# Kernel tuning notes

Hardware: AMD Instinct MI355X
Metric: run time of the kernel (lower is better)

The kernel has to match this reference:

```python
import jax, jax.numpy as jnp
import numpy as np

ALPHA = 0.5

def setup_inputs() -> dict:
    key = jax.random.key(0)
    k1, k2 = jax.random.split(key)
    B, S, F_IN, F_OUT = 64, 512, 1024, 1024
    x = jax.random.normal(k1, (B, S, F_IN), dtype=jnp.float32)
    W = jax.random.normal(k2, (F_OUT, F_IN), dtype=jnp.float32) * (F_IN ** -0.5)
    return {"x": x, "W": W}

def reference(x, W):
    # x: [B, S, F_in], W: [F_out, F_in] (torch Linear layout, no bias)
    alpha = jnp.asarray(ALPHA, dtype=x.dtype)
    # Project all segments at once (the big GEMM), then scan the EMA recurrence.
    y = jnp.einsum('bsf,of->bso', x, W)  # [B, S, F_out]
    y_t = jnp.swapaxes(y, 0, 1)          # [S, B, F_out] for scan over segments

    def step(h, yk):
        h = alpha * h + (1 - alpha) * yk
        return h, h

    h0 = jnp.zeros((x.shape[0], W.shape[0]), dtype=x.dtype)
    hk, hiddens_t = jax.lax.scan(step, h0, y_t)
    hiddens = jnp.swapaxes(hiddens_t, 0, 1)  # [B, S, F_out]
    return (hk, hiddens)
```

## Files before the change

kernel.cpp:

```cpp
#include <hip/hip_runtime.h>
#include <hip/hip_bf16.h>
#include <stdint.h>

#define B_DIM 64
#define S_DIM 512
#define K_DIM 1024
#define N_DIM 1024
#define M_DIM (B_DIM * S_DIM)

typedef __attribute__((ext_vector_type(8))) short short8;
typedef __attribute__((ext_vector_type(4))) float floatx4;

__global__ __launch_bounds__(256) void scan_x_kernel(
    const float* __restrict__ x, __hip_bfloat16* __restrict__ xs) {
  const int t  = blockIdx.x * 256 + threadIdx.x;
  const int f4 = (t & 255) << 2;
  const int c  = (t >> 8) & 15;
  const int b  = t >> 12;
  const size_t base = (size_t)b * S_DIM * K_DIM + f4;
  const int s0 = c * 32;

  float4 h = {0.f, 0.f, 0.f, 0.f};
  if (c != 0) {
    #pragma unroll 8
    for (int s = s0 - 16; s < s0; ++s) {
      float4 v = *(const float4*)(x + base + (size_t)s * K_DIM);
      h.x = 0.5f * (h.x + v.x); h.y = 0.5f * (h.y + v.y);
      h.z = 0.5f * (h.z + v.z); h.w = 0.5f * (h.w + v.w);
    }
  }
  #pragma unroll 8
  for (int s = s0; s < s0 + 32; ++s) {
    float4 v = *(const float4*)(x + base + (size_t)s * K_DIM);
    h.x = 0.5f * (h.x + v.x); h.y = 0.5f * (h.y + v.y);
    h.z = 0.5f * (h.z + v.z); h.w = 0.5f * (h.w + v.w);
    __hip_bfloat16 b0 = __float2bfloat16(h.x);
    __hip_bfloat16 b1 = __float2bfloat16(h.y);
    __hip_bfloat16 b2 = __float2bfloat16(h.z);
    __hip_bfloat16 b3 = __float2bfloat16(h.w);
    union { unsigned short u[4]; uint2 v2; } pk;
    pk.u[0] = *(unsigned short*)&b0; pk.u[1] = *(unsigned short*)&b1;
    pk.u[2] = *(unsigned short*)&b2; pk.u[3] = *(unsigned short*)&b3;
    *(uint2*)(xs + base + (size_t)s * K_DIM) = pk.v2;
  }
}

__global__ __launch_bounds__(256) void conv_w_kernel(
    const float* __restrict__ W, __hip_bfloat16* __restrict__ Wb) {
  int t = blockIdx.x * 256 + threadIdx.x;
  Wb[t] = __float2bfloat16(W[t]);
}

__global__ __launch_bounds__(256) void gemm_kernel(
    const __hip_bfloat16* __restrict__ A,
    const __hip_bfloat16* __restrict__ Bw,
    float* __restrict__ out) {
  __shared__ __hip_bfloat16 lA[128 * 64];
  __shared__ __hip_bfloat16 lB[128 * 64];

  const int tid  = threadIdx.x;
  const int lane = tid & 63;
  const int w    = tid >> 6;
  const int wm   = (w >> 1) * 64;
  const int wn   = (w & 1) * 64;
  const int quad = lane >> 4;
  const int l15  = lane & 15;
  const int r7   = l15 & 7;

  const int bi    = blockIdx.x;
  const int xcd   = bi & 7;
  const int local = bi >> 3;
  const int m0 = (xcd * 32 + (local >> 3)) * 128;
  const int n0 = (local & 7) * 128;

  floatx4 acc[4][4] = {};

  for (int k0 = 0; k0 < K_DIM; k0 += 64) {
    #pragma unroll
    for (int p = 0; p < 4; ++p) {
      int c    = tid + p * 256;
      int r    = c >> 3;
      int slot = c & 7;
      int kc   = (slot ^ (r & 7)) * 8;
      const __hip_bfloat16* ga = A  + (size_t)(m0 + r) * K_DIM + k0 + kc;
      const __hip_bfloat16* gb = Bw + (size_t)(n0 + r) * K_DIM + k0 + kc;
      __builtin_amdgcn_global_load_lds(
          (const __attribute__((address_space(1))) void*)ga,
          (__attribute__((address_space(3))) void*)&lA[c * 8], 16, 0, 0);
      __builtin_amdgcn_global_load_lds(
          (const __attribute__((address_space(1))) void*)gb,
          (__attribute__((address_space(3))) void*)&lB[c * 8], 16, 0, 0);
    }
    __syncthreads();

    #pragma unroll
    for (int kk = 0; kk < 64; kk += 32) {
      const int q0 = kk >> 3;
      short8 af[4], bfr[4];
      #pragma unroll
      for (int i = 0; i < 4; ++i) {
        af[i]  = *(const short8*)&lA[(wm + i * 16 + l15) * 64 +
                                     (((q0 + quad) ^ r7) * 8)];
        bfr[i] = *(const short8*)&lB[(wn + i * 16 + l15) * 64 +
                                     (((q0 + quad) ^ r7) * 8)];
      }
      #pragma unroll
      for (int i = 0; i < 4; ++i)
        #pragma unroll
        for (int j = 0; j < 4; ++j)
          acc[i][j] = __builtin_amdgcn_mfma_f32_16x16x32_bf16(
              af[i], bfr[j], acc[i][j], 0, 0, 0);
    }
    __syncthreads();
  }

  float* hid = out + B_DIM * N_DIM;
  #pragma unroll
  for (int i = 0; i < 4; ++i) {
    #pragma unroll
    for (int j = 0; j < 4; ++j) {
      #pragma unroll
      for (int r = 0; r < 4; ++r) {
        int gm = m0 + wm + i * 16 + quad * 4 + r;
        int gn = n0 + wn + j * 16 + l15;
        float v = acc[i][j][r];
        hid[(size_t)gm * N_DIM + gn] = v;
        if ((gm & (S_DIM - 1)) == (S_DIM - 1)) {
          out[(size_t)(gm >> 9) * N_DIM + gn] = v;
        }
      }
    }
  }
}

extern "C" void kernel_launch(void* const* d_in, const int* in_sizes, int n_in,
                              void* d_out, int out_size, void* d_ws, size_t ws_size,
                              hipStream_t stream) {
  const float* x = (const float*)d_in[0];
  const float* W = (const float*)d_in[1];
  float* out = (float*)d_out;

  __hip_bfloat16* xs = (__hip_bfloat16*)d_ws;
  __hip_bfloat16* Wb = (__hip_bfloat16*)((char*)d_ws + (size_t)M_DIM * K_DIM * 2);

  scan_x_kernel<<<dim3(262144 / 256), dim3(256), 0, stream>>>(x, xs);
  conv_w_kernel<<<dim3((N_DIM * K_DIM) / 256), dim3(256), 0, stream>>>(W, Wb);
  gemm_kernel<<<dim3((M_DIM / 128) * (N_DIM / 128)), dim3(256), 0, stream>>>(xs, Wb, out);
}
```

Measured before the change: 332.9 us.

## Move EMA scan into GEMM epilogue with warm-start states instead of prescanning x

Replaces the strided per-column EMA prescan of x with a plain vectorized fp32-to-bf16 conversion, and applies the recurrence to GEMM outputs inside the epilogue. It uses lane shuffles across MFMA quads, an LDS handoff between waves, and a small warm-start GEMM that seeds each 128-row tile with a truncated 16-step history. This swaps the serial, poorly coalesced scan pass over x for a streaming conversion plus extra epilogue arithmetic, one more launch and a tiny GEMM. The truncated warm start and tiny decay factors are approximations, as in the old prescan.

```diff
diff --git a/kernel.cpp b/kernel.cpp
--- a/kernel.cpp
+++ b/kernel.cpp
@@ -7,56 +7,81 @@
 #define K_DIM 1024
 #define N_DIM 1024
 #define M_DIM (B_DIM * S_DIM)
+#define N_TILES 256
 
 typedef __attribute__((ext_vector_type(8))) short short8;
 typedef __attribute__((ext_vector_type(4))) float floatx4;
 
-__global__ __launch_bounds__(256) void scan_x_kernel(
+__device__ __forceinline__ uint4 pack8_bf16(float4 a, float4 b) {
+  union { unsigned short u[8]; uint4 q; } pk;
+  __hip_bfloat16 t;
+  t = __float2bfloat16(a.x); pk.u[0] = *(unsigned short*)&t;
+  t = __float2bfloat16(a.y); pk.u[1] = *(unsigned short*)&t;
+  t = __float2bfloat16(a.z); pk.u[2] = *(unsigned short*)&t;
+  t = __float2bfloat16(a.w); pk.u[3] = *(unsigned short*)&t;
+  t = __float2bfloat16(b.x); pk.u[4] = *(unsigned short*)&t;
+  t = __float2bfloat16(b.y); pk.u[5] = *(unsigned short*)&t;
+  t = __float2bfloat16(b.z); pk.u[6] = *(unsigned short*)&t;
+  t = __float2bfloat16(b.w); pk.u[7] = *(unsigned short*)&t;
+  return pk.q;
+}
+
+__global__ __launch_bounds__(256) void conv_x_kernel(
     const float* __restrict__ x, __hip_bfloat16* __restrict__ xs) {
-  const int t  = blockIdx.x * 256 + threadIdx.x;
-  const int f4 = (t & 255) << 2;
-  const int c  = (t >> 8) & 15;
-  const int b  = t >> 12;
-  const size_t base = (size_t)b * S_DIM * K_DIM + f4;
-  const int s0 = c * 32;
-
-  float4 h = {0.f, 0.f, 0.f, 0.f};
-  if (c != 0) {
-    #pragma unroll 8
-    for (int s = s0 - 16; s < s0; ++s) {
-      float4 v = *(const float4*)(x + base + (size_t)s * K_DIM);
-      h.x = 0.5f * (h.x + v.x); h.y = 0.5f * (h.y + v.y);
-      h.z = 0.5f * (h.z + v.z); h.w = 0.5f * (h.w + v.w);
-    }
-  }
-  #pragma unroll 8
-  for (int s = s0; s < s0 + 32; ++s) {
-    float4 v = *(const float4*)(x + base + (size_t)s * K_DIM);
-    h.x = 0.5f * (h.x + v.x); h.y = 0.5f * (h.y + v.y);
-    h.z = 0.5f * (h.z + v.z); h.w = 0.5f * (h.w + v.w);
-    __hip_bfloat16 b0 = __float2bfloat16(h.x);
-    __hip_bfloat16 b1 = __float2bfloat16(h.y);
-    __hip_bfloat16 b2 = __float2bfloat16(h.z);
-    __hip_bfloat16 b3 = __float2bfloat16(h.w);
-    union { unsigned short u[4]; uint2 v2; } pk;
-    pk.u[0] = *(unsigned short*)&b0; pk.u[1] = *(unsigned short*)&b1;
-    pk.u[2] = *(unsigned short*)&b2; pk.u[3] = *(unsigned short*)&b3;
-    *(uint2*)(xs + base + (size_t)s * K_DIM) = pk.v2;
+  const size_t stride = 2048u * 256u;
+  size_t t = (size_t)blockIdx.x * 256 + threadIdx.x;
+  #pragma unroll
+  for (int it = 0; it < 8; ++it, t += stride) {
+    float4 v0 = *(const float4*)(x + t * 8);
+    float4 v1 = *(const float4*)(x + t * 8 + 4);
+    *(uint4*)(xs + t * 8) = pack8_bf16(v0, v1);
   }
 }
 
 __global__ __launch_bounds__(256) void conv_w_kernel(
     const float* __restrict__ W, __hip_bfloat16* __restrict__ Wb) {
-  int t = blockIdx.x * 256 + threadIdx.x;
-  Wb[t] = __float2bfloat16(W[t]);
-}
-
-__global__ __launch_bounds__(256) void gemm_kernel(
+  const size_t t = (size_t)blockIdx.x * 256 + threadIdx.x;
+  float4 v0 = *(const float4*)(W + t * 8);
+  float4 v1 = *(const float4*)(W + t * 8 + 4);
+  *(uint4*)(Wb + t * 8) = pack8_bf16(v0, v1);
+}
+
+__global__ __launch_bounds__(256) void wx_kernel(
+    const float* __restrict__ x, __hip_bfloat16* __restrict__ wx) {
+  const int t = blockIdx.x;
+  const int b = t >> 2;
+  const int c = t & 3;
+  const int k4 = threadIdx.x * 4;
+  float4 acc = {0.f, 0.f, 0.f, 0.f};
+  if (c != 0) {
+    const float* base = x + ((size_t)b * S_DIM + c * 128) * K_DIM + k4;
+    float wgt = 0.5f;
+    #pragma unroll
+    for (int j = 1; j <= 16; ++j) {
+      float4 v = *(const float4*)(base - (size_t)j * K_DIM);
+      acc.x += wgt * v.x; acc.y += wgt * v.y;
+      acc.z += wgt * v.z; acc.w += wgt * v.w;
+      wgt *= 0.5f;
+    }
+  }
+  union { unsigned short u[4]; uint2 q; } pk;
+  __hip_bfloat16 h;
+  h = __float2bfloat16(acc.x); pk.u[0] = *(unsigned short*)&h;
+  h = __float2bfloat16(acc.y); pk.u[1] = *(unsigned short*)&h;
+  h = __float2bfloat16(acc.z); pk.u[2] = *(unsigned short*)&h;
+  h = __float2bfloat16(acc.w); pk.u[3] = *(unsigned short*)&h;
+  *(uint2*)(wx + (size_t)t * K_DIM + k4) = pk.q;
+}
+
+template <bool MAIN>
+__global__ __launch_bounds__(256) void gemm_tmpl(
     const __hip_bfloat16* __restrict__ A,
     const __hip_bfloat16* __restrict__ Bw,
-    float* __restrict__ out) {
+    float* __restrict__ out,
+    const float* __restrict__ warm) {
   __shared__ __hip_bfloat16 lA[128 * 64];
   __shared__ __hip_bfloat16 lB[128 * 64];
+  __shared__ float hbuf[128];
 
   const int tid  = threadIdx.x;
   const int lane = tid & 63;
@@ -67,11 +92,17 @@
   const int l15  = lane & 15;
   const int r7   = l15 & 7;
 
-  const int bi    = blockIdx.x;
-  const int xcd   = bi & 7;
-  const int local = bi >> 3;
-  const int m0 = (xcd * 32 + (local >> 3)) * 128;
-  const int n0 = (local & 7) * 128;
+  int m0, n0;
+  if (MAIN) {
+    const int bi    = blockIdx.x;
+    const int xcd   = bi & 7;
+    const int local = bi >> 3;
+    m0 = (xcd * 32 + (local >> 3)) * 128;
+    n0 = (local & 7) * 128;
+  } else {
+    m0 = (blockIdx.x >> 3) * 128;
+    n0 = (blockIdx.x & 7) * 128;
+  }
 
   floatx4 acc[4][4] = {};
 
@@ -114,7 +145,62 @@
     __syncthreads();
   }
 
-  float* hid = out + B_DIM * N_DIM;
+  if (MAIN) {
+    const float fq = (quad == 0) ? 1.f : (quad == 1) ? 0.0625f
+                   : (quad == 2) ? 0.00390625f : 2.44140625e-4f;
+    const int tile = m0 >> 7;
+    #pragma unroll
+    for (int j = 0; j < 4; ++j) {
+      const int colIdx = wn + j * 16 + l15;
+      float Wst = 0.f;
+      if (w < 2) Wst = warm[(size_t)tile * N_DIM + n0 + colIdx];
+      #pragma unroll
+      for (int i = 0; i < 4; ++i) {
+        const float y0 = acc[i][j][0], y1 = acc[i][j][1];
+        const float y2 = acc[i][j][2], y3 = acc[i][j][3];
+        const float L0 = 0.5f * y0;
+        const float L1 = 0.5f * (L0 + y1);
+        const float L2 = 0.5f * (L1 + y2);
+        const float L3 = 0.5f * (L2 + y3);
+        float P = L3;
+        float t1 = __shfl_up(P, 16);
+        if (quad >= 1) P += 0.0625f * t1;
+        float t2 = __shfl_up(P, 32);
+        if (quad >= 2) P += 0.00390625f * t2;
+        float H = __shfl_up(P, 16);
+        H = (quad >= 1) ? H : 0.f;
+        const float S = H + fq * Wst;
+        acc[i][j][0] = L0 + 0.5f    * S;
+        acc[i][j][1] = L1 + 0.25f   * S;
+        acc[i][j][2] = L2 + 0.125f  * S;
+        acc[i][j][3] = L3 + 0.0625f * S;
+        const float F = __shfl(P, 48 + l15);
+        Wst = F + 1.52587890625e-05f * Wst;
+      }
+      if (w < 2 && quad == 0) hbuf[colIdx] = Wst;
+    }
+    __syncthreads();
+    if (w >= 2) {
+      #pragma unroll
+      for (int j = 0; j < 4; ++j) {
+        const float Z = hbuf[wn + j * 16 + l15] * fq;
+        #pragma unroll
+        for (int i = 0; i < 4; ++i) {
+          const float fi = (i == 0) ? 1.f
+                         : (i == 1) ? 1.52587890625e-05f
+                         : (i == 2) ? 2.3283064365386963e-10f
+                                    : 3.552713678800501e-15f;
+          const float base = fi * Z;
+          acc[i][j][0] += 0.5f    * base;
+          acc[i][j][1] += 0.25f   * base;
+          acc[i][j][2] += 0.125f  * base;
+          acc[i][j][3] += 0.0625f * base;
+        }
+      }
+    }
+  }
+
+  float* hid = MAIN ? out + B_DIM * N_DIM : out;
   #pragma unroll
   for (int i = 0; i < 4; ++i) {
     #pragma unroll
@@ -125,7 +211,7 @@
         int gn = n0 + wn + j * 16 + l15;
         float v = acc[i][j][r];
         hid[(size_t)gm * N_DIM + gn] = v;
-        if ((gm & (S_DIM - 1)) == (S_DIM - 1)) {
+        if (MAIN && ((gm & (S_DIM - 1)) == (S_DIM - 1))) {
           out[(size_t)(gm >> 9) * N_DIM + gn] = v;
         }
       }
@@ -141,9 +227,13 @@
   float* out = (float*)d_out;
 
   __hip_bfloat16* xs = (__hip_bfloat16*)d_ws;
-  __hip_bfloat16* Wb = (__hip_bfloat16*)((char*)d_ws + (size_t)M_DIM * K_DIM * 2);
-
-  scan_x_kernel<<<dim3(262144 / 256), dim3(256), 0, stream>>>(x, xs);
-  conv_w_kernel<<<dim3((N_DIM * K_DIM) / 256), dim3(256), 0, stream>>>(W, Wb);
-  gemm_kernel<<<dim3((M_DIM / 128) * (N_DIM / 128)), dim3(256), 0, stream>>>(xs, Wb, out);
-}
+  __hip_bfloat16* Wb = xs + (size_t)M_DIM * K_DIM;
+  __hip_bfloat16* wx = Wb + (size_t)N_DIM * K_DIM;
+  float*          wy = (float*)(wx + (size_t)N_TILES * K_DIM);
+
+  conv_x_kernel<<<dim3(2048), dim3(256), 0, stream>>>(x, xs);
+  conv_w_kernel<<<dim3((N_DIM * K_DIM) / (256 * 8)), dim3(256), 0, stream>>>(W, Wb);
+  wx_kernel<<<dim3(N_TILES), dim3(256), 0, stream>>>(x, wx);
+  gemm_tmpl<false><<<dim3(16), dim3(256), 0, stream>>>(wx, Wb, wy, nullptr);
+  gemm_tmpl<true><<<dim3((M_DIM / 128) * (N_DIM / 128)), dim3(256), 0, stream>>>(xs, Wb, out, wy);
+}
```

After: 344.1 us. 1.03x slower.
